# Kernel optimization log

Hardware: AMD Instinct MI355X
Metric: run time of the kernel (lower is better)

The kernel has to match this reference:

```python
import jax, jax.numpy as jnp
import numpy as np

LN_EPS = 1e-12


def setup_inputs() -> dict:
    key = jax.random.key(0)
    ks = jax.random.split(key, 5)
    B, N, D_IN, D_OUT, E = 32, 2048, 128, 128, 64
    return {
        "x": jax.random.normal(ks[0], (B, N, D_IN), dtype=jnp.float32),
        "node_embeddings": jax.random.normal(ks[1], (N, E), dtype=jnp.float32),
        "time_embeddings": jax.random.normal(ks[2], (E,), dtype=jnp.float32),
        "weights_pool": jax.random.normal(ks[3], (E, 2, D_IN, D_OUT), dtype=jnp.float32) * 0.02,
        "bias_pool": jax.random.normal(ks[4], (E, D_OUT), dtype=jnp.float32) * 0.02,
        "ln_weight": jnp.ones((E,), dtype=jnp.float32),
        "ln_bias": jnp.zeros((E,), dtype=jnp.float32),
    }


def reference(x, node_embeddings, time_embeddings, weights_pool, bias_pool, ln_weight, ln_bias):
    # e: [N, E] = LayerNorm(node_emb + time_emb)  (dropout in eval mode = identity)
    e = node_embeddings + time_embeddings[None, :]
    mu = jnp.mean(e, axis=-1, keepdims=True)
    var = jnp.mean(jnp.square(e - mu), axis=-1, keepdims=True)
    e = (e - mu) * jax.lax.rsqrt(var + LN_EPS) * ln_weight + ln_bias

    # adaptive adjacency: softmax over rows of e @ e.T  -> [N, N]
    adj = jax.nn.softmax(jnp.einsum('nd,md->nm', e, e), axis=1)

    # per-node weights [N, 2, I, O] and bias [N, O]
    weights = jnp.einsum('nd,dkio->nkio', e, weights_pool)
    bias = e @ bias_pool  # [N, O]

    # supports: k=0 identity (x itself), k=1 adjacency aggregation
    x_agg = jnp.einsum('nm,bmc->bnc', adj, x)        # [B, N, I]
    x_g = jnp.stack([x, x_agg], axis=2)              # [B, N, 2, I]

    # per-node batched GEMM + bias
    out = jnp.einsum('bnki,nkio->bno', x_g, weights) + bias
    return out
```

## Files before the change

kernel.cpp:

```cpp
#include <hip/hip_runtime.h>


typedef unsigned short u16;
typedef unsigned int u32;
typedef __attribute__((ext_vector_type(8))) short bf16x8;
typedef __attribute__((ext_vector_type(4))) float f32x4;
typedef const __attribute__((address_space(1))) u16* gas1;
typedef __attribute__((address_space(3))) u16* las3;

#define NN 2048
#define EE 64
#define CC 128
#define BB 32

__device__ __forceinline__ u16 f2bf(float f) {
  u32 u = __builtin_bit_cast(u32, f);
  u += 0x7fffu + ((u >> 16) & 1u);
  return (u16)(u >> 16);
}

__device__ __forceinline__ f32x4 mfma16(bf16x8 a, bf16x8 b, f32x4 c) {
  return __builtin_amdgcn_mfma_f32_16x16x32_bf16(a, b, c, 0, 0, 0);
}

__global__ __launch_bounds__(64) void k_prep(
    const float* __restrict__ ne, const float* __restrict__ te,
    const float* __restrict__ lnw, const float* __restrict__ lnb,
    const float* __restrict__ bias_pool,
    float* __restrict__ e, u16* __restrict__ e_bf, float* __restrict__ bias_out) {
  int n = blockIdx.x;
  int d = threadIdx.x;
  float v = ne[n * EE + d] + te[d];
  float s = v;
#pragma unroll
  for (int off = 32; off > 0; off >>= 1) s += __shfl_xor(s, off);
  float mean = s * (1.0f / 64.0f);
  float c = v - mean;
  float q = c * c;
#pragma unroll
  for (int off = 32; off > 0; off >>= 1) q += __shfl_xor(q, off);
  float inv = rsqrtf(q * (1.0f / 64.0f) + 1e-12f);
  float ev = c * inv * lnw[d] + lnb[d];
  e[n * EE + d] = ev;
  e_bf[n * EE + d] = f2bf(ev);
  __shared__ float sh[64];
  sh[d] = ev;
  __syncthreads();
#pragma unroll
  for (int oo = 0; oo < 2; ++oo) {
    int o = oo * 64 + d;
    float acc = 0.f;
#pragma unroll 8
    for (int dd = 0; dd < 64; ++dd) acc += sh[dd] * bias_pool[dd * CC + o];
    bias_out[n * CC + o] = acc;
  }
}

__global__ __launch_bounds__(256) void k_poolt(const float* __restrict__ pool,
                                               u16* __restrict__ pool_r) {
  __shared__ float t[128 * 65];
  int ki = blockIdx.x;
  int tid = threadIdx.x;
  for (int it = 0; it < 32; ++it) {
    int idx = it * 256 + tid;
    int d = idx >> 7, o = idx & 127;
    t[o * 65 + d] = pool[d * 32768 + ki * 128 + o];
  }
  __syncthreads();
  for (int it = 0; it < 32; ++it) {
    int idx = it * 256 + tid;
    int o = idx >> 6, d = idx & 63;
    pool_r[((size_t)o * 256 + ki) * 64 + d] = f2bf(t[o * 65 + d]);
  }
}

__global__ __launch_bounds__(256) void k_xtrans(const float* __restrict__ x,
                                                u16* __restrict__ x_t,
                                                u16* __restrict__ xg_t) {
  __shared__ u16 t[128 * 68];
  int b = blockIdx.x >> 5;
  int m0 = (blockIdx.x & 31) * 64;
  int tid = threadIdx.x;
  for (int it = 0; it < 32; ++it) {
    int idx = it * 256 + tid;
    int m = idx >> 7, c = idx & 127;
    float v = x[((size_t)b * NN + m0 + m) * CC + c];
    t[c * 68 + m] = f2bf(v);
  }
  __syncthreads();
  for (int it = 0; it < 32; ++it) {
    int idx = it * 256 + tid;
    int c = idx >> 6, m = idx & 63;
    x_t[((size_t)b * CC + c) * NN + m0 + m] = t[c * 68 + m];
  }
  for (int it = 0; it < 16; ++it) {
    int idx = it * 256 + tid;
    int m = idx >> 6, c2 = idx & 63;
    float2 v = *(const float2*)&x[((size_t)b * NN + m0 + m) * CC + c2 * 2];
    u32 pk = (u32)f2bf(v.x) | ((u32)f2bf(v.y) << 16);
    *(u32*)&xg_t[(((size_t)(m0 + m)) * 32 + b) * 256 + c2 * 2] = pk;
  }
}

__global__ __launch_bounds__(256) void k_S(const float* __restrict__ e,
                                           float* __restrict__ S) {
  extern __shared__ float sm[];
  float* er = sm;
  float* ec = sm + 128 * 68;
  int n0 = (blockIdx.x >> 4) * 128, m0 = (blockIdx.x & 15) * 128;
  int tid = threadIdx.x;
  for (int it = 0; it < 32; ++it) {
    int idx = it * 256 + tid;
    int r = idx >> 6, d = idx & 63;
    er[r * 68 + d] = e[(n0 + r) * EE + d];
    ec[r * 68 + d] = e[(m0 + r) * EE + d];
  }
  __syncthreads();
  int tx = tid & 15, ty = tid >> 4;
  float acc[8][8] = {};
  for (int d4 = 0; d4 < 64; d4 += 4) {
    f32x4 av[8], bv[8];
#pragma unroll
    for (int i = 0; i < 8; ++i) av[i] = *(const f32x4*)&er[(ty + 16 * i) * 68 + d4];
#pragma unroll
    for (int j = 0; j < 8; ++j) bv[j] = *(const f32x4*)&ec[(tx + 16 * j) * 68 + d4];
#pragma unroll
    for (int i = 0; i < 8; ++i)
#pragma unroll
      for (int j = 0; j < 8; ++j) {
        acc[i][j] += av[i][0] * bv[j][0];
        acc[i][j] += av[i][1] * bv[j][1];
        acc[i][j] += av[i][2] * bv[j][2];
        acc[i][j] += av[i][3] * bv[j][3];
      }
  }
#pragma unroll
  for (int i = 0; i < 8; ++i)
#pragma unroll
    for (int j = 0; j < 8; ++j)
      S[(size_t)(n0 + ty + 16 * i) * NN + m0 + tx + 16 * j] = acc[i][j];
}

__global__ __launch_bounds__(256) void k_softmax(const float* __restrict__ S,
                                                 u16* __restrict__ adj) {
  int n = blockIdx.x;
  int tid = threadIdx.x;
  int lane = tid & 63, w = tid >> 6;
  __shared__ float red[8];
  const f32x4* Srow = (const f32x4*)(S + (size_t)n * NN);
  f32x4 v0 = Srow[tid];
  f32x4 v1 = Srow[256 + tid];
  float mx = v0[0];
#pragma unroll
  for (int k = 1; k < 4; ++k) mx = fmaxf(mx, v0[k]);
#pragma unroll
  for (int k = 0; k < 4; ++k) mx = fmaxf(mx, v1[k]);
#pragma unroll
  for (int off = 32; off > 0; off >>= 1) mx = fmaxf(mx, __shfl_xor(mx, off));
  if (lane == 0) red[w] = mx;
  __syncthreads();
  mx = fmaxf(fmaxf(red[0], red[1]), fmaxf(red[2], red[3]));
  float ex[8];
  float sum = 0.f;
#pragma unroll
  for (int k = 0; k < 4; ++k) { ex[k] = __expf(v0[k] - mx); sum += ex[k]; }
#pragma unroll
  for (int k = 0; k < 4; ++k) { ex[4 + k] = __expf(v1[k] - mx); sum += ex[4 + k]; }
#pragma unroll
  for (int off = 32; off > 0; off >>= 1) sum += __shfl_xor(sum, off);
  if (lane == 0) red[4 + w] = sum;
  __syncthreads();
  sum = red[4] + red[5] + red[6] + red[7];
  float rs = 1.0f / sum;
  u16* arow = adj + (size_t)n * NN;
  u32 p0 = (u32)f2bf(ex[0] * rs) | ((u32)f2bf(ex[1] * rs) << 16);
  u32 p1 = (u32)f2bf(ex[2] * rs) | ((u32)f2bf(ex[3] * rs) << 16);
  ((uint2*)arow)[tid] = make_uint2(p0, p1);
  p0 = (u32)f2bf(ex[4] * rs) | ((u32)f2bf(ex[5] * rs) << 16);
  p1 = (u32)f2bf(ex[6] * rs) | ((u32)f2bf(ex[7] * rs) << 16);
  ((uint2*)arow)[256 + tid] = make_uint2(p0, p1);
}

__global__ __launch_bounds__(256, 3) void k_aggr(const u16* __restrict__ adj,
                                                 const u16* __restrict__ x_t,
                                                 u16* __restrict__ xg_t) {
  __shared__ u16 As[128 * 64];
  __shared__ u16 Bs[128 * 64];
  int mb = blockIdx.x & 15, b = blockIdx.x >> 4;
  int n0 = mb * 128;
  int tid = threadIdx.x;
  int lane = tid & 63, w = tid >> 6;
  int wm = w >> 1, wn = w & 1;
  int lm = lane & 15, lq = lane >> 4;
  f32x4 acc[4][4] = {};
  const u16* a_src = adj + (size_t)n0 * NN;
  const u16* b_src = x_t + (size_t)b * CC * NN;
  for (int kc = 0; kc < NN; kc += 64) {
    __syncthreads();
#pragma unroll
    for (int ii = 0; ii < 4; ++ii) {
      int idx = ii * 256 + tid;
      int row = idx >> 3, ch = idx & 7;
      __builtin_amdgcn_global_load_lds((gas1)(a_src + (size_t)row * NN + kc + ch * 8),
                                       (las3)(As + (size_t)(ii * 256 + w * 64) * 8), 16, 0, 0);
      __builtin_amdgcn_global_load_lds((gas1)(b_src + (size_t)row * NN + kc + ch * 8),
                                       (las3)(Bs + (size_t)(ii * 256 + w * 64) * 8), 16, 0, 0);
    }
    __syncthreads();
#pragma unroll
    for (int kk = 0; kk < 64; kk += 32) {
      bf16x8 af[4], bq[4];
#pragma unroll
      for (int i = 0; i < 4; ++i)
        af[i] = *(const bf16x8*)&As[(wm * 64 + i * 16 + lm) * 64 + kk + lq * 8];
#pragma unroll
      for (int j = 0; j < 4; ++j)
        bq[j] = *(const bf16x8*)&Bs[(wn * 64 + j * 16 + lm) * 64 + kk + lq * 8];
#pragma unroll
      for (int i = 0; i < 4; ++i)
#pragma unroll
        for (int j = 0; j < 4; ++j)
          acc[i][j] = mfma16(af[i], bq[j], acc[i][j]);
    }
  }
#pragma unroll
  for (int i = 0; i < 4; ++i) {
    int nr = n0 + wm * 64 + i * 16 + lq * 4;
#pragma unroll
    for (int j = 0; j < 4; ++j) {
      int c = wn * 64 + j * 16 + lm;
#pragma unroll
      for (int r = 0; r < 4; ++r)
        xg_t[((size_t)(nr + r) * 32 + b) * 256 + 128 + c] = f2bf(acc[i][j][r]);
    }
  }
}

__global__ __launch_bounds__(256, 4) void k_out(const u16* __restrict__ e_bf,
                                                const u16* __restrict__ pool_r,
                                                const u16* __restrict__ xg_t,
                                                const float* __restrict__ bias,
                                                float* __restrict__ out) {
  __shared__ u16 Wl[16 * 1040];
  int ng = blockIdx.x & 127, og = blockIdx.x >> 7;
  int n0 = ng * 16, o0 = og * 16;
  int tid = threadIdx.x;
  int lane = tid & 63, w = tid >> 6;
  int lm = lane & 15, lq = lane >> 4;

  bf16x8 eF0 = *(const bf16x8*)&e_bf[(n0 + lm) * EE + lq * 8];
  bf16x8 eF1 = *(const bf16x8*)&e_bf[(n0 + lm) * EE + 32 + lq * 8];
  f32x4 acc[4][2] = {};

  for (int c = 0; c < 4; ++c) {
    int t = c * 4 + w;
#pragma unroll 8
    for (int o = 0; o < 16; ++o) {
      const u16* ap = pool_r + ((size_t)(o0 + o) * 256 + t * 16 + lm) * 64 + lq * 8;
      bf16x8 p0 = *(const bf16x8*)ap;
      bf16x8 p1 = *(const bf16x8*)(ap + 32);
      f32x4 g = {0.f, 0.f, 0.f, 0.f};
      g = mfma16(p0, eF0, g);
      g = mfma16(p1, eF1, g);
      ushort4 h;
      h.x = f2bf(g[0]); h.y = f2bf(g[1]); h.z = f2bf(g[2]); h.w = f2bf(g[3]);
      *(ushort4*)&Wl[lm * 1040 + o * 64 + w * 16 + lq * 4] = h;
    }
    __syncthreads();
#pragma unroll
    for (int nn = 0; nn < 4; ++nn) {
      int nd = w * 4 + nn;
      int n = n0 + nd;
#pragma unroll
      for (int ks = 0; ks < 2; ++ks) {
        int kloc = c * 64 + ks * 32 + lq * 8;
        bf16x8 a0 = *(const bf16x8*)&xg_t[((size_t)n * 32 + lm) * 256 + kloc];
        bf16x8 a1 = *(const bf16x8*)&xg_t[((size_t)n * 32 + 16 + lm) * 256 + kloc];
        bf16x8 bv = *(const bf16x8*)&Wl[nd * 1040 + lm * 64 + ks * 32 + lq * 8];
        acc[nn][0] = mfma16(a0, bv, acc[nn][0]);
        acc[nn][1] = mfma16(a1, bv, acc[nn][1]);
      }
    }
    __syncthreads();
  }

#pragma unroll
  for (int nn = 0; nn < 4; ++nn) {
    int n = n0 + w * 4 + nn;
    int oc = o0 + lm;
    float bv = bias[n * CC + oc];
#pragma unroll
    for (int mt = 0; mt < 2; ++mt)
#pragma unroll
      for (int r = 0; r < 4; ++r) {
        int b = mt * 16 + lq * 4 + r;
        out[((size_t)b * NN + n) * CC + oc] = acc[nn][mt][r] + bv;
      }
  }
}

extern "C" void kernel_launch(void* const* d_in, const int* in_sizes, int n_in,
                              void* d_out, int out_size, void* d_ws, size_t ws_size,
                              hipStream_t stream) {
  const float* x        = (const float*)d_in[0];
  const float* node_emb = (const float*)d_in[1];
  const float* time_emb = (const float*)d_in[2];
  const float* pool     = (const float*)d_in[3];
  const float* bias_pl  = (const float*)d_in[4];
  const float* ln_w     = (const float*)d_in[5];
  const float* ln_b     = (const float*)d_in[6];
  float* out = (float*)d_out;

  char* p = (char*)d_ws;
  auto alloc = [&](size_t bytes) {
    char* r = p;
    p += (bytes + 255) & ~(size_t)255;
    return r;
  };
  float* e      = (float*)alloc((size_t)NN * EE * 4);
  u16*   e_bf   = (u16*)  alloc((size_t)NN * EE * 2);
  float* biasb  = (float*)alloc((size_t)NN * CC * 4);
  u16*   adj    = (u16*)  alloc((size_t)NN * NN * 2);
  u16*   x_t    = (u16*)  alloc((size_t)BB * CC * NN * 2);
  u16*   xg_t   = (u16*)  alloc((size_t)NN * BB * 256 * 2);
  u16*   pool_r = (u16*)  alloc((size_t)128 * 256 * 64 * 2);
  float* S      = (float*)alloc((size_t)NN * NN * 4);

  if (ws_size < (size_t)(p - (char*)d_ws)) return;

  (void)hipFuncSetAttribute((const void*)k_S, hipFuncAttributeMaxDynamicSharedMemorySize,
                            2 * 128 * 68 * 4);

  k_prep<<<NN, 64, 0, stream>>>(node_emb, time_emb, ln_w, ln_b, bias_pl, e, e_bf, biasb);
  k_poolt<<<256, 256, 0, stream>>>(pool, pool_r);
  k_xtrans<<<BB * 32, 256, 0, stream>>>(x, x_t, xg_t);
  k_S<<<256, 256, 2 * 128 * 68 * 4, stream>>>(e, S);
  k_softmax<<<NN, 256, 0, stream>>>(S, adj);
  k_aggr<<<16 * BB, 256, 0, stream>>>(adj, x_t, xg_t);
  k_out<<<8 * 128, 256, 0, stream>>>(e_bf, pool_r, xg_t, biasb, out);
}
```

Measured before the change: 277.7 us.

## Split fused per-node weight generation into separate generate and apply kernels

The fused k_out kernel, which generated per-node weights into shared memory and applied them per output tile, is replaced by two kernels. k_gen materializes all per-node weights (N x 2*I*O in bf16, about 128 MB) to global memory as a dense MFMA GEMM of e against pool. k_apply then runs a per-node 32x256x128 GEMM that reads those weights back. This removes the shared-memory staging and barriers of the fused design, in exchange for a large extra global write and read of the weight tensor and a big new workspace allocation.

```diff
diff --git a/kernel.cpp b/kernel.cpp
--- a/kernel.cpp
+++ b/kernel.cpp
@@ -236,65 +236,78 @@
   }
 }
 
-__global__ __launch_bounds__(256, 4) void k_out(const u16* __restrict__ e_bf,
-                                                const u16* __restrict__ pool_r,
-                                                const u16* __restrict__ xg_t,
-                                                const float* __restrict__ bias,
-                                                float* __restrict__ out) {
-  __shared__ u16 Wl[16 * 1040];
-  int ng = blockIdx.x & 127, og = blockIdx.x >> 7;
-  int n0 = ng * 16, o0 = og * 16;
+__global__ __launch_bounds__(256) void k_gen(const u16* __restrict__ e_bf,
+                                             const u16* __restrict__ pool_r,
+                                             u16* __restrict__ W_t) {
+  int cb = blockIdx.x & 255, nb = blockIdx.x >> 8;
+  int c0 = cb * 128, n0 = nb * 64;
   int tid = threadIdx.x;
   int lane = tid & 63, w = tid >> 6;
   int lm = lane & 15, lq = lane >> 4;
-
-  bf16x8 eF0 = *(const bf16x8*)&e_bf[(n0 + lm) * EE + lq * 8];
-  bf16x8 eF1 = *(const bf16x8*)&e_bf[(n0 + lm) * EE + 32 + lq * 8];
-  f32x4 acc[4][2] = {};
-
-  for (int c = 0; c < 4; ++c) {
-    int t = c * 4 + w;
-#pragma unroll 8
-    for (int o = 0; o < 16; ++o) {
-      const u16* ap = pool_r + ((size_t)(o0 + o) * 256 + t * 16 + lm) * 64 + lq * 8;
-      bf16x8 p0 = *(const bf16x8*)ap;
-      bf16x8 p1 = *(const bf16x8*)(ap + 32);
-      f32x4 g = {0.f, 0.f, 0.f, 0.f};
-      g = mfma16(p0, eF0, g);
-      g = mfma16(p1, eF1, g);
+  bf16x8 eB[4][2];
+#pragma unroll
+  for (int nt = 0; nt < 4; ++nt)
+#pragma unroll
+    for (int ks = 0; ks < 2; ++ks)
+      eB[nt][ks] = *(const bf16x8*)&e_bf[(n0 + nt * 16 + lm) * EE + ks * 32 + lq * 8];
+  f32x4 acc[2][4] = {};
+#pragma unroll
+  for (int ct = 0; ct < 2; ++ct)
+#pragma unroll
+    for (int ks = 0; ks < 2; ++ks) {
+      bf16x8 pA = *(const bf16x8*)&pool_r[
+          ((size_t)c0 + (w * 2 + ct) * 16 + lm) * 64 + ks * 32 + lq * 8];
+#pragma unroll
+      for (int nt = 0; nt < 4; ++nt)
+        acc[ct][nt] = mfma16(pA, eB[nt][ks], acc[ct][nt]);
+    }
+#pragma unroll
+  for (int ct = 0; ct < 2; ++ct)
+#pragma unroll
+    for (int nt = 0; nt < 4; ++nt) {
+      int node = n0 + nt * 16 + lm;
+      int col = c0 + (w * 2 + ct) * 16 + lq * 4;
       ushort4 h;
-      h.x = f2bf(g[0]); h.y = f2bf(g[1]); h.z = f2bf(g[2]); h.w = f2bf(g[3]);
-      *(ushort4*)&Wl[lm * 1040 + o * 64 + w * 16 + lq * 4] = h;
-    }
-    __syncthreads();
-#pragma unroll
-    for (int nn = 0; nn < 4; ++nn) {
-      int nd = w * 4 + nn;
-      int n = n0 + nd;
-#pragma unroll
-      for (int ks = 0; ks < 2; ++ks) {
-        int kloc = c * 64 + ks * 32 + lq * 8;
-        bf16x8 a0 = *(const bf16x8*)&xg_t[((size_t)n * 32 + lm) * 256 + kloc];
-        bf16x8 a1 = *(const bf16x8*)&xg_t[((size_t)n * 32 + 16 + lm) * 256 + kloc];
-        bf16x8 bv = *(const bf16x8*)&Wl[nd * 1040 + lm * 64 + ks * 32 + lq * 8];
-        acc[nn][0] = mfma16(a0, bv, acc[nn][0]);
-        acc[nn][1] = mfma16(a1, bv, acc[nn][1]);
-      }
-    }
-    __syncthreads();
-  }
-
-#pragma unroll
-  for (int nn = 0; nn < 4; ++nn) {
-    int n = n0 + w * 4 + nn;
-    int oc = o0 + lm;
+      h.x = f2bf(acc[ct][nt][0]); h.y = f2bf(acc[ct][nt][1]);
+      h.z = f2bf(acc[ct][nt][2]); h.w = f2bf(acc[ct][nt][3]);
+      *(ushort4*)&W_t[(size_t)node * 32768 + col] = h;
+    }
+}
+
+__global__ __launch_bounds__(256, 3) void k_apply(const u16* __restrict__ xg_t,
+                                                  const u16* __restrict__ W_t,
+                                                  const float* __restrict__ bias,
+                                                  float* __restrict__ out) {
+  int n0 = blockIdx.x * 2;
+  int tid = threadIdx.x;
+  int lane = tid & 63, w = tid >> 6;
+  int lm = lane & 15, lq = lane >> 4;
+  int n = n0 + (w & 1), oh = w >> 1;
+  const u16* xb = xg_t + (size_t)n * 32 * 256;
+  const u16* wb = W_t + (size_t)n * 32768 + (size_t)oh * 64 * 256;
+  f32x4 acc[2][4] = {};
+#pragma unroll
+  for (int ks = 0; ks < 8; ++ks) {
+    int ko = ks * 32 + lq * 8;
+    bf16x8 a0 = *(const bf16x8*)&xb[lm * 256 + ko];
+    bf16x8 a1 = *(const bf16x8*)&xb[(16 + lm) * 256 + ko];
+#pragma unroll
+    for (int ot = 0; ot < 4; ++ot) {
+      bf16x8 bv = *(const bf16x8*)&wb[(ot * 16 + lm) * 256 + ko];
+      acc[0][ot] = mfma16(a0, bv, acc[0][ot]);
+      acc[1][ot] = mfma16(a1, bv, acc[1][ot]);
+    }
+  }
+#pragma unroll
+  for (int ot = 0; ot < 4; ++ot) {
+    int oc = oh * 64 + ot * 16 + lm;
     float bv = bias[n * CC + oc];
 #pragma unroll
     for (int mt = 0; mt < 2; ++mt)
 #pragma unroll
       for (int r = 0; r < 4; ++r) {
         int b = mt * 16 + lq * 4 + r;
-        out[((size_t)b * NN + n) * CC + oc] = acc[nn][mt][r] + bv;
+        out[((size_t)b * NN + n) * CC + oc] = acc[mt][ot][r] + bv;
       }
   }
 }
@@ -325,6 +338,7 @@
   u16*   xg_t   = (u16*)  alloc((size_t)NN * BB * 256 * 2);
   u16*   pool_r = (u16*)  alloc((size_t)128 * 256 * 64 * 2);
   float* S      = (float*)alloc((size_t)NN * NN * 4);
+  u16*   W_t    = (u16*)  alloc((size_t)NN * 32768 * 2);
 
   if (ws_size < (size_t)(p - (char*)d_ws)) return;
 
@@ -334,8 +348,9 @@
   k_prep<<<NN, 64, 0, stream>>>(node_emb, time_emb, ln_w, ln_b, bias_pl, e, e_bf, biasb);
   k_poolt<<<256, 256, 0, stream>>>(pool, pool_r);
   k_xtrans<<<BB * 32, 256, 0, stream>>>(x, x_t, xg_t);
+  k_gen<<<256 * 32, 256, 0, stream>>>(e_bf, pool_r, W_t);
   k_S<<<256, 256, 2 * 128 * 68 * 4, stream>>>(e, S);
   k_softmax<<<NN, 256, 0, stream>>>(S, adj);
   k_aggr<<<16 * BB, 256, 0, stream>>>(adj, x_t, xg_t);
-  k_out<<<8 * 128, 256, 0, stream>>>(e_bf, pool_r, xg_t, biasb, out);
-}
+  k_apply<<<NN / 2, 256, 0, stream>>>(xg_t, W_t, biasb, out);
+}
```

Result: slower. 299.7 us (+7.9%).
